# Kernel optimization log

Measured on AMD Instinct MI355X. Metric: run time of the kernel, lower is better.

Reference implementation:

```python
import jax, jax.numpy as jnp
import numpy as np

B, S, IN, HID, HEADS, TRAITS = 128, 32, 32, 128, 8, 10


def setup_inputs() -> dict:
    key = jax.random.key(0)
    ks = jax.random.split(key, 40)
    f32 = jnp.float32
    def W(k, shape, s=0.02):
        return (jax.random.normal(k, shape, f32) * s)
    path = jax.random.normal(ks[0], (B, S, IN), f32)
    # monotonically increasing shared time grid (timestamps[0] is what cdeint uses)
    dt = jax.random.uniform(ks[1], (S,), f32, 0.05, 0.15)
    ts = jnp.broadcast_to(jnp.cumsum(dt), (B, S))
    inp = {
        "interaction_path": path,
        "timestamps": ts,
        # initial encoder: Linear(IN,HID) -> LN -> GELU -> Linear(HID,HID) -> LN
        "enc_W1": W(ks[2], (IN, HID)), "enc_b1": jnp.zeros((HID,), f32),
        "enc_g1": jnp.ones((HID,), f32), "enc_bt1": jnp.zeros((HID,), f32),
        "enc_W2": W(ks[3], (HID, HID)), "enc_b2": jnp.zeros((HID,), f32),
        "enc_g2": jnp.ones((HID,), f32), "enc_bt2": jnp.zeros((HID,), f32),
        # vector field: Linear(HID,2HID)->LN->GELU -> Linear(2HID,2HID)->LN->GELU -> Linear(2HID,HID*IN)
        "vf_W1": W(ks[4], (HID, 2 * HID)), "vf_b1": jnp.zeros((2 * HID,), f32),
        "vf_g1": jnp.ones((2 * HID,), f32), "vf_bt1": jnp.zeros((2 * HID,), f32),
        "vf_W2": W(ks[5], (2 * HID, 2 * HID)), "vf_b2": jnp.zeros((2 * HID,), f32),
        "vf_g2": jnp.ones((2 * HID,), f32), "vf_bt2": jnp.zeros((2 * HID,), f32),
        "vf_W3": W(ks[6], (2 * HID, HID * IN), 0.005), "vf_b3": jnp.zeros((HID * IN,), f32),
        # MultiheadAttention (q=k=v, single token)
        "Wq": W(ks[7], (HID, HID)), "bq": jnp.zeros((HID,), f32),
        "Wk": W(ks[8], (HID, HID)), "bk": jnp.zeros((HID,), f32),
        "Wv": W(ks[9], (HID, HID)), "bv": jnp.zeros((HID,), f32),
        "Wo": W(ks[10], (HID, HID)), "bo": jnp.zeros((HID,), f32),
        # trait decoder (2-layer MLP -> TRAITS)
        "dec_W1": W(ks[11], (HID, HID)), "dec_b1": jnp.zeros((HID,), f32),
        "dec_W2": W(ks[12], (HID, TRAITS)), "dec_b2": jnp.zeros((TRAITS,), f32),
    }
    return inp


def reference(interaction_path, timestamps,
              enc_W1, enc_b1, enc_g1, enc_bt1, enc_W2, enc_b2, enc_g2, enc_bt2,
              vf_W1, vf_b1, vf_g1, vf_bt1, vf_W2, vf_b2, vf_g2, vf_bt2, vf_W3, vf_b3,
              Wq, bq, Wk, bk, Wv, bv, Wo, bo,
              dec_W1, dec_b1, dec_W2, dec_b2):
    b, s, in_dim = interaction_path.shape
    hid = enc_W1.shape[1]
    nh = HEADS
    dh = hid // nh

    def ln(x, g, bb):
        mu = jnp.mean(x, -1, keepdims=True)
        v = jnp.mean((x - mu) ** 2, -1, keepdims=True)
        return (x - mu) / jnp.sqrt(v + 1e-5) * g + bb

    gelu = lambda x: jax.nn.gelu(x, approximate=False)

    # initial encoder on first time point (dropout = eval mode)
    x0 = interaction_path[:, 0]
    h0 = gelu(ln(x0 @ enc_W1 + enc_b1, enc_g1, enc_bt1))
    z0 = ln(h0 @ enc_W2 + enc_b2, enc_g2, enc_bt2)  # [B, HID]

    # linear-interpolation control path: piecewise-constant derivative per interval
    dts = timestamps[:, 1:] - timestamps[:, :-1]                       # [B, S-1]
    dX = (interaction_path[:, 1:] - interaction_path[:, :-1]) / dts[..., None]  # [B, S-1, IN]

    def vf(z):
        h = gelu(ln(z @ vf_W1 + vf_b1, vf_g1, vf_bt1))
        h = gelu(ln(h @ vf_W2 + vf_b2, vf_g2, vf_bt2))
        return (h @ vf_W3 + vf_b3).reshape(z.shape[0], hid, in_dim)    # [B, HID, IN]

    def drift(z, dxdt):
        return jnp.einsum('bhi,bi->bh', vf(z), dxdt)

    def rk4_step(z, inp):
        dxdt, hstep = inp               # [B, IN], [B]
        hb = hstep[:, None]
        k1 = drift(z, dxdt)
        k2 = drift(z + 0.5 * hb * k1, dxdt)
        k3 = drift(z + 0.5 * hb * k2, dxdt)
        k4 = drift(z + hb * k3, dxdt)
        z_next = z + (hb / 6.0) * (k1 + 2 * k2 + 2 * k3 + k4)
        return z_next, None

    zT, _ = jax.lax.scan(rk4_step, z0, (jnp.swapaxes(dX, 0, 1), dts.T))  # [B, HID]

    # single-token self-attention (softmax over one key -> weights = 1)
    q = (zT @ Wq + bq).reshape(b, nh, dh)
    k = (zT @ Wk + bk).reshape(b, nh, dh)
    v = (zT @ Wv + bv).reshape(b, nh, dh)
    scores = jnp.sum(q * k, -1, keepdims=True) / jnp.sqrt(jnp.float32(dh))  # [B, nh, 1]
    w = jax.nn.softmax(scores[..., None], axis=-1)                           # [B, nh, 1, 1] == 1
    attn = (w[..., 0] * v).reshape(b, hid)
    final = attn @ Wo + bo
    attention_weights = jnp.mean(w, axis=1)  # [B, 1, 1] averaged over heads (torch default)

    hD = gelu(final @ dec_W1 + dec_b1)
    traits = hD @ dec_W2 + dec_b2            # [B, TRAITS]
    return traits, attention_weights
```

## Files before the change

kernel.cpp:

```cpp
#include <hip/hip_runtime.h>
#include <hip/hip_bf16.h>

#define BB 128
#define SS 32
#define NSTEP 31
#define IND 32
#define HID 128
#define HID2 256

typedef unsigned short u16;
typedef unsigned int u32;
typedef _Float16 f16;
typedef f16 h2 __attribute__((ext_vector_type(2)));
typedef __fp16 fp16v2 __attribute__((ext_vector_type(2)));
typedef _Float16 f16x8 __attribute__((ext_vector_type(8)));
typedef float f32x4 __attribute__((ext_vector_type(4)));

__device__ __forceinline__ float dot2f(u32 a, u32 b, float c){
#if __has_builtin(__builtin_amdgcn_fdot2)
  h2 ha, hb; __builtin_memcpy(&ha, &a, 4); __builtin_memcpy(&hb, &b, 4);
  return __builtin_amdgcn_fdot2(ha, hb, c, false);
#else
  h2 ha, hb; __builtin_memcpy(&ha, &a, 4); __builtin_memcpy(&hb, &b, 4);
  return c + (float)ha[0]*(float)hb[0] + (float)ha[1]*(float)hb[1];
#endif
}
__device__ __forceinline__ u32 pkh2(float a, float b){
  fp16v2 r = __builtin_amdgcn_cvt_pkrtz(a, b);
  u32 u; __builtin_memcpy(&u, &r, 4); return u;
}
__device__ __forceinline__ u16 f2h(float f){ f16 h = (f16)f; u16 u; __builtin_memcpy(&u, &h, 2); return u; }
__device__ __forceinline__ float gelu_f(float x){ return 0.5f * x * (1.0f + erff(x * 0.70710678118654752440f)); }

__device__ __forceinline__ float wred(float v){
  int iv; float tf;
  #define DPPADD(CTRL, RMASK) \
    __builtin_memcpy(&iv, &v, 4); \
    iv = __builtin_amdgcn_update_dpp(0, iv, CTRL, RMASK, 0xf, true); \
    __builtin_memcpy(&tf, &iv, 4); \
    v += tf;
  DPPADD(0x111, 0xf)
  DPPADD(0x112, 0xf)
  DPPADD(0x114, 0xf)
  DPPADD(0x118, 0xf)
  DPPADD(0x142, 0xa)
  DPPADD(0x143, 0xc)
  #undef DPPADD
  return v;
}

__device__ __forceinline__ void bsum2(float x, float y, float* red, int tid, float& ox, float& oy){
  #pragma unroll
  for (int off = 32; off >= 1; off >>= 1){ x += __shfl_xor(x, off); y += __shfl_xor(y, off); }
  __syncthreads();
  if ((tid & 63) == 0){ red[(tid >> 6)*2] = x; red[(tid >> 6)*2 + 1] = y; }
  __syncthreads();
  ox = red[0] + red[2] + red[4] + red[6];
  oy = red[1] + red[3] + red[5] + red[7];
}

__global__ __launch_bounds__(128) void prep_misc(const float* __restrict__ path,
                                                 const float* __restrict__ ts,
                                                 const float* __restrict__ b3,
                                                 u32* __restrict__ dxh,
                                                 float* __restrict__ hb,
                                                 float* __restrict__ gb){
  const int b = blockIdx.x, tid = threadIdx.x;
  __shared__ float sdx[NSTEP * IND];
  for (int t = tid; t < NSTEP * IND; t += 128){
    int s = t >> 5, i = t & 31;
    float dt = ts[b*SS + s + 1] - ts[b*SS + s];
    sdx[t] = (path[(b*SS + s + 1)*IND + i] - path[(b*SS + s)*IND + i]) / dt;
  }
  if (tid < NSTEP) hb[b*NSTEP + tid] = ts[b*SS + tid + 1] - ts[b*SS + tid];
  __syncthreads();
  for (int t = tid; t < NSTEP * 16; t += 128){
    int s = t >> 4, i2 = t & 15;
    dxh[((size_t)b*NSTEP + s)*16 + i2] = pkh2(sdx[s*IND + 2*i2], sdx[s*IND + 2*i2 + 1]);
  }
  if (tid < HID){
    float w[IND];
    #pragma unroll
    for (int i = 0; i < IND; ++i) w[i] = b3[tid*IND + i];
    for (int s = 0; s < NSTEP; ++s){
      float a = 0.f;
      #pragma unroll
      for (int i = 0; i < IND; ++i) a = fmaf(w[i], sdx[s*IND + i], a);
      gb[(b*NSTEP + s)*HID + tid] = a;
    }
  }
}

__global__ __launch_bounds__(256) void pack_w3(const float* __restrict__ W3, u32* __restrict__ w3h){
  int i = blockIdx.x*256 + threadIdx.x;
  if (i < (HID2*HID*IND)/2) w3h[i] = pkh2(W3[2*i], W3[2*i + 1]);
}

__global__ __launch_bounds__(256) void pack_wf(const float* __restrict__ W1,
                                               const float* __restrict__ W2,
                                               u32* __restrict__ w1f,
                                               u32* __restrict__ w2f){
  int i = blockIdx.x*256 + threadIdx.x;
  if (i < 16384){
    int lane_blk = i >> 6, rem = i & 63;
    int i16 = rem >> 2, q = rem & 3;
    int w = lane_blk >> 6, lane = lane_blk & 63;
    int kt = i16 >> 2, nt = i16 & 3;
    int k = kt*32 + (lane >> 4)*8 + 2*q;
    int col = w*64 + nt*16 + (lane & 15);
    w1f[i] = pkh2(W1[(size_t)k*HID2 + col], W1[(size_t)(k+1)*HID2 + col]);
  } else if (i < 16384 + 32768){
    int j = i - 16384;
    int lane_blk = j >> 7, rem = j & 127;
    int i32i = rem >> 2, q = rem & 3;
    int w = lane_blk >> 6, lane = lane_blk & 63;
    int kt = i32i >> 2, nt = i32i & 3;
    int k = kt*32 + (lane >> 4)*8 + 2*q;
    int col = w*64 + nt*16 + (lane & 15);
    w2f[j] = pkh2(W2[(size_t)k*HID2 + col], W2[(size_t)(k+1)*HID2 + col]);
  }
}

__global__ __launch_bounds__(256) void gprep_h(const u32* __restrict__ w3h,
                                               const u32* __restrict__ dxh,
                                               u32* __restrict__ Gp, int s0){
  const int tid = threadIdx.x;
  const int sl = blockIdx.y; const int s = s0 + sl;
  const int lin = blockIdx.x*256 + tid;
  const int kp = lin >> 7, h = lin & 127;
  const uint4* wa = (const uint4*)(w3h + ((size_t)(2*kp)*HID + h)*16);
  const uint4* wb = (const uint4*)(w3h + ((size_t)(2*kp+1)*HID + h)*16);
  uint4 A0 = wa[0], A1 = wa[1], A2 = wa[2], A3 = wa[3];
  uint4 B0 = wb[0], B1 = wb[1], B2 = wb[2], B3 = wb[3];
  __shared__ u32 sdx[BB * 16];
  for (int t = tid; t < BB * 16; t += 256){
    int bb = t >> 4, i2 = t & 15;
    sdx[t] = dxh[((size_t)bb*NSTEP + s)*16 + i2];
  }
  __syncthreads();
  const int kt = kp >> 4, q = kp & 3, quad2 = (kp >> 2) & 3;
  const int wq = h >> 5, tq = (h >> 4) & 1, nn = h & 15;
  const size_t off = (size_t)wq*4096 + (size_t)(kt*2 + tq)*256 + (size_t)(quad2*16 + nn)*4 + q;
  const size_t base_sl = (size_t)sl * BB * 16384;
  for (int bb = 0; bb < BB; ++bb){
    const uint4* dp = (const uint4*)&sdx[bb*16];
    uint4 D0 = dp[0], D1 = dp[1], D2 = dp[2], D3 = dp[3];
    float g0 = 0.f, g1 = 0.f, g2 = 0.f, g3 = 0.f;
    g0 = dot2f(D0.x, A0.x, g0); g0 = dot2f(D0.y, A0.y, g0);
    g0 = dot2f(D0.z, A0.z, g0); g0 = dot2f(D0.w, A0.w, g0);
    g2 = dot2f(D1.x, A1.x, g2); g2 = dot2f(D1.y, A1.y, g2);
    g2 = dot2f(D1.z, A1.z, g2); g2 = dot2f(D1.w, A1.w, g2);
    g0 = dot2f(D2.x, A2.x, g0); g0 = dot2f(D2.y, A2.y, g0);
    g0 = dot2f(D2.z, A2.z, g0); g0 = dot2f(D2.w, A2.w, g0);
    g2 = dot2f(D3.x, A3.x, g2); g2 = dot2f(D3.y, A3.y, g2);
    g2 = dot2f(D3.z, A3.z, g2); g2 = dot2f(D3.w, A3.w, g2);
    g1 = dot2f(D0.x, B0.x, g1); g1 = dot2f(D0.y, B0.y, g1);
    g1 = dot2f(D0.z, B0.z, g1); g1 = dot2f(D0.w, B0.w, g1);
    g3 = dot2f(D1.x, B1.x, g3); g3 = dot2f(D1.y, B1.y, g3);
    g3 = dot2f(D1.z, B1.z, g3); g3 = dot2f(D1.w, B1.w, g3);
    g1 = dot2f(D2.x, B2.x, g1); g1 = dot2f(D2.y, B2.y, g1);
    g1 = dot2f(D2.z, B2.z, g1); g1 = dot2f(D2.w, B2.w, g1);
    g3 = dot2f(D3.x, B3.x, g3); g3 = dot2f(D3.y, B3.y, g3);
    g3 = dot2f(D3.z, B3.z, g3); g3 = dot2f(D3.w, B3.w, g3);
    Gp[base_sl + (size_t)bb*16384 + off] = pkh2(g0 + g2, g1 + g3);
  }
}

struct ScanP {
  const float *path;
  const float *eW1,*eb1,*eg1,*ebt1,*eW2,*eb2,*eg2,*ebt2;
  const u32 *w1f, *w2f;
  const float *b1,*g1,*bt1,*b2,*g2,*bt2;
  const float *Wv,*bv,*Wo,*bo,*dW1,*db1,*dW2,*db2;
  const float *hb,*gb;
  const u32 *Gp;
  float *zstate, *out;
  int s0, s1, do_enc, do_epi;
};

__global__ __launch_bounds__(256, 1) void scan_kernel(ScanP p){
  const int tid = threadIdx.x;
  const int b = blockIdx.x;
  const int lane = tid & 63, w = tid >> 6;
  const int quad = lane >> 4, n16 = lane & 15;
  const bool owner = (quad == 0);
  __shared__ __align__(16) u16 zst_h[HID];
  __shared__ __align__(16) u16 a1p_h[HID2];
  __shared__ __align__(16) u16 a2p_h[HID2];
  __shared__ __align__(16) float red[8];
  __shared__ __align__(16) float zf[HID];
  __shared__ __align__(16) float sc1[HID2];

  uint4 w1r[16], w2r[32];
  {
    const uint4* s1p = (const uint4*)p.w1f + ((size_t)(w*64 + lane))*16;
    #pragma unroll
    for (int i = 0; i < 16; ++i) w1r[i] = s1p[i];
    const uint4* s2p = (const uint4*)p.w2f + ((size_t)(w*64 + lane))*32;
    #pragma unroll
    for (int i = 0; i < 32; ++i) w2r[i] = s2p[i];
  }
  float rb1[4], rg1[4], rbt1[4], rb2[4], rg2[4], rbt2[4];
  #pragma unroll
  for (int nt = 0; nt < 4; ++nt){
    int col = w*64 + nt*16 + n16;
    rb1[nt] = p.b1[col]; rg1[nt] = p.g1[col]; rbt1[nt] = p.bt1[col];
    rb2[nt] = p.b2[col]; rg2[nt] = p.g2[col]; rbt2[nt] = p.bt2[col];
  }
  const int h0 = w*32 + n16, h1 = h0 + 16;

  float mu, sq;
  if (p.do_enc){
    if (tid < IND) sc1[tid] = p.path[(b*SS + 0)*IND + tid];
    __syncthreads();
    float acc = 0.f;
    if (tid < HID){
      acc = p.eb1[tid];
      #pragma unroll 8
      for (int i = 0; i < IND; ++i) acc = fmaf(sc1[i], p.eW1[i*HID + tid], acc);
    }
    float cx = (tid < HID) ? acc : 0.f;
    bsum2(cx, cx*cx, red, tid, mu, sq);
    mu *= (1.f/HID); float var = sq*(1.f/HID) - mu*mu; float rstd = rsqrtf(var + 1e-5f);
    if (tid < HID) zf[tid] = gelu_f((acc - mu)*rstd*p.eg1[tid] + p.ebt1[tid]);
    __syncthreads();
    float acc2 = 0.f;
    if (tid < HID){
      acc2 = p.eb2[tid];
      #pragma unroll 8
      for (int h = 0; h < HID; ++h) acc2 = fmaf(zf[h], p.eW2[h*HID + tid], acc2);
    }
    cx = (tid < HID) ? acc2 : 0.f;
    bsum2(cx, cx*cx, red, tid, mu, sq);
    mu *= (1.f/HID); float var2 = sq*(1.f/HID) - mu*mu; float rstd2 = rsqrtf(var2 + 1e-5f);
    __syncthreads();
    if (tid < HID) zf[tid] = (acc2 - mu)*rstd2*p.eg2[tid] + p.ebt2[tid];
    __syncthreads();
  }
  float zc0 = 0.f, zc1 = 0.f;
  if (owner){
    if (p.do_enc){ zc0 = zf[h0]; zc1 = zf[h1]; }
    else { zc0 = p.zstate[b*HID + h0]; zc1 = p.zstate[b*HID + h1]; }
  }

  for (int s = p.s0; s < p.s1; ++s){
    const float hbv = p.hb[b*NSTEP + s];
    uint4 gr[16];
    {
      const uint4* g4 = (const uint4*)(p.Gp + ((size_t)(s - p.s0)*BB + b)*16384 + (size_t)w*4096);
      #pragma unroll
      for (int m = 0; m < 16; ++m) gr[m] = g4[m*64 + lane];
    }
    float gb0 = 0.f, gb1 = 0.f;
    if (owner){
      gb0 = p.gb[(b*NSTEP + s)*HID + h0];
      gb1 = p.gb[(b*NSTEP + s)*HID + h1];
      zst_h[h0] = f2h(zc0); zst_h[h1] = f2h(zc1);
    }
    float ks0 = 0.f, ks1 = 0.f;
    __syncthreads();

    #pragma unroll 1
    for (int st = 0; st < 4; ++st){
      f32x4 D0 = {0,0,0,0}, D1 = {0,0,0,0}, D2 = {0,0,0,0}, D3 = {0,0,0,0};
      {
        const uint4* za = (const uint4*)zst_h;
        #pragma unroll
        for (int kt = 0; kt < 4; ++kt){
          f16x8 a; uint4 av = za[kt*4 + quad]; __builtin_memcpy(&a, &av, 16);
          f16x8 bf;
          __builtin_memcpy(&bf, &w1r[kt*4+0], 16); D0 = __builtin_amdgcn_mfma_f32_16x16x32_f16(a, bf, D0, 0, 0, 0);
          __builtin_memcpy(&bf, &w1r[kt*4+1], 16); D1 = __builtin_amdgcn_mfma_f32_16x16x32_f16(a, bf, D1, 0, 0, 0);
          __builtin_memcpy(&bf, &w1r[kt*4+2], 16); D2 = __builtin_amdgcn_mfma_f32_16x16x32_f16(a, bf, D2, 0, 0, 0);
          __builtin_memcpy(&bf, &w1r[kt*4+3], 16); D3 = __builtin_amdgcn_mfma_f32_16x16x32_f16(a, bf, D3, 0, 0, 0);
        }
      }
      float v0 = D0[0] + rb1[0], v1 = D1[0] + rb1[1], v2 = D2[0] + rb1[2], v3 = D3[0] + rb1[3];
      float ssum = wred((v0 + v1) + (v2 + v3));
      float ssq  = wred((v0*v0 + v1*v1) + (v2*v2 + v3*v3));
      if (lane == 63){ red[w*2] = ssum; red[w*2+1] = ssq; }
      __syncthreads();
      {
        const float4* r4 = (const float4*)red;
        float4 ra = r4[0], rb = r4[1];
        float m1 = (ra.x + ra.z + rb.x + rb.z)*(1.f/1024.f);
        float q1 = (ra.y + ra.w + rb.y + rb.w)*(1.f/1024.f);
        float rs1 = rsqrtf(q1 - m1*m1 + 1e-5f);
        if (owner){
          a1p_h[w*64 +  0 + n16] = f2h(gelu_f((v0 - m1)*rs1*rg1[0] + rbt1[0]));
          a1p_h[w*64 + 16 + n16] = f2h(gelu_f((v1 - m1)*rs1*rg1[1] + rbt1[1]));
          a1p_h[w*64 + 32 + n16] = f2h(gelu_f((v2 - m1)*rs1*rg1[2] + rbt1[2]));
          a1p_h[w*64 + 48 + n16] = f2h(gelu_f((v3 - m1)*rs1*rg1[3] + rbt1[3]));
        }
      }
      __syncthreads();
      D0 = {0,0,0,0}; D1 = {0,0,0,0}; D2 = {0,0,0,0}; D3 = {0,0,0,0};
      {
        const uint4* aa = (const uint4*)a1p_h;
        #pragma unroll
        for (int kt = 0; kt < 8; ++kt){
          f16x8 a; uint4 av = aa[kt*4 + quad]; __builtin_memcpy(&a, &av, 16);
          f16x8 bf;
          __builtin_memcpy(&bf, &w2r[kt*4+0], 16); D0 = __builtin_amdgcn_mfma_f32_16x16x32_f16(a, bf, D0, 0, 0, 0);
          __builtin_memcpy(&bf, &w2r[kt*4+1], 16); D1 = __builtin_amdgcn_mfma_f32_16x16x32_f16(a, bf, D1, 0, 0, 0);
          __builtin_memcpy(&bf, &w2r[kt*4+2], 16); D2 = __builtin_amdgcn_mfma_f32_16x16x32_f16(a, bf, D2, 0, 0, 0);
          __builtin_memcpy(&bf, &w2r[kt*4+3], 16); D3 = __builtin_amdgcn_mfma_f32_16x16x32_f16(a, bf, D3, 0, 0, 0);
        }
      }
      v0 = D0[0] + rb2[0]; v1 = D1[0] + rb2[1]; v2 = D2[0] + rb2[2]; v3 = D3[0] + rb2[3];
      ssum = wred((v0 + v1) + (v2 + v3));
      ssq  = wred((v0*v0 + v1*v1) + (v2*v2 + v3*v3));
      if (lane == 63){ red[w*2] = ssum; red[w*2+1] = ssq; }
      __syncthreads();
      {
        const float4* r4 = (const float4*)red;
        float4 ra = r4[0], rb = r4[1];
        float m2 = (ra.x + ra.z + rb.x + rb.z)*(1.f/1024.f);
        float q2 = (ra.y + ra.w + rb.y + rb.w)*(1.f/1024.f);
        float rs2 = rsqrtf(q2 - m2*m2 + 1e-5f);
        if (owner){
          a2p_h[w*64 +  0 + n16] = f2h(gelu_f((v0 - m2)*rs2*rg2[0] + rbt2[0]));
          a2p_h[w*64 + 16 + n16] = f2h(gelu_f((v1 - m2)*rs2*rg2[1] + rbt2[1]));
          a2p_h[w*64 + 32 + n16] = f2h(gelu_f((v2 - m2)*rs2*rg2[2] + rbt2[2]));
          a2p_h[w*64 + 48 + n16] = f2h(gelu_f((v3 - m2)*rs2*rg2[3] + rbt2[3]));
        }
      }
      __syncthreads();
      f32x4 E0 = {0,0,0,0}, E1 = {0,0,0,0};
      {
        const uint4* aa = (const uint4*)a2p_h;
        #pragma unroll
        for (int kt = 0; kt < 8; ++kt){
          f16x8 a; uint4 av = aa[kt*4 + quad]; __builtin_memcpy(&a, &av, 16);
          f16x8 g0f, g1f;
          __builtin_memcpy(&g0f, &gr[kt*2+0], 16);
          __builtin_memcpy(&g1f, &gr[kt*2+1], 16);
          E0 = __builtin_amdgcn_mfma_f32_16x16x32_f16(a, g0f, E0, 0, 0, 0);
          E1 = __builtin_amdgcn_mfma_f32_16x16x32_f16(a, g1f, E1, 0, 0, 0);
        }
      }
      if (owner){
        float kv0 = E0[0] + gb0, kv1 = E1[0] + gb1;
        float cst = (st == 0 || st == 3) ? 1.f : 2.f;
        ks0 += cst*kv0; ks1 += cst*kv1;
        if (st < 3){
          float c = (st == 2) ? hbv : 0.5f*hbv;
          zst_h[h0] = f2h(zc0 + c*kv0);
          zst_h[h1] = f2h(zc1 + c*kv1);
        }
      }
      __syncthreads();
    }
    if (owner){ zc0 += hbv*(1.f/6.f)*ks0; zc1 += hbv*(1.f/6.f)*ks1; }
  }

  if (p.do_epi){
    if (owner){ zf[h0] = zc0; zf[h1] = zc1; }
    __syncthreads();
    if (tid < HID){
      float v = p.bv[tid];
      #pragma unroll 8
      for (int h = 0; h < HID; ++h) v = fmaf(zf[h], p.Wv[h*HID + tid], v);
      sc1[tid] = v;
    }
    __syncthreads();
    if (tid < HID){
      float f = p.bo[tid];
      #pragma unroll 8
      for (int h = 0; h < HID; ++h) f = fmaf(sc1[h], p.Wo[h*HID + tid], f);
      sc1[HID + tid] = f;
    }
    __syncthreads();
    if (tid < HID){
      float hd = p.db1[tid];
      #pragma unroll 8
      for (int h = 0; h < HID; ++h) hd = fmaf(sc1[HID + h], p.dW1[h*HID + tid], hd);
      zf[tid] = gelu_f(hd);
    }
    __syncthreads();
    if (tid < 10){
      float t = p.db2[tid];
      #pragma unroll 8
      for (int h = 0; h < HID; ++h) t = fmaf(zf[h], p.dW2[h*10 + tid], t);
      p.out[b*10 + tid] = t;
    }
    if (tid == 0) p.out[BB*10 + b] = 1.0f;
  } else {
    if (owner){ p.zstate[b*HID + h0] = zc0; p.zstate[b*HID + h1] = zc1; }
  }
}

extern "C" void kernel_launch(void* const* d_in, const int* in_sizes, int n_in,
                              void* d_out, int out_size, void* d_ws, size_t ws_size,
                              hipStream_t stream){
  const float* path  = (const float*)d_in[0];
  const float* ts    = (const float*)d_in[1];
  const float* eW1   = (const float*)d_in[2];
  const float* eb1   = (const float*)d_in[3];
  const float* eg1   = (const float*)d_in[4];
  const float* ebt1  = (const float*)d_in[5];
  const float* eW2   = (const float*)d_in[6];
  const float* eb2   = (const float*)d_in[7];
  const float* eg2   = (const float*)d_in[8];
  const float* ebt2  = (const float*)d_in[9];
  const float* vW1   = (const float*)d_in[10];
  const float* vb1   = (const float*)d_in[11];
  const float* vg1   = (const float*)d_in[12];
  const float* vbt1  = (const float*)d_in[13];
  const float* vW2   = (const float*)d_in[14];
  const float* vb2   = (const float*)d_in[15];
  const float* vg2   = (const float*)d_in[16];
  const float* vbt2  = (const float*)d_in[17];
  const float* vW3   = (const float*)d_in[18];
  const float* vb3   = (const float*)d_in[19];
  const float* Wv    = (const float*)d_in[24];
  const float* bv    = (const float*)d_in[25];
  const float* Wo    = (const float*)d_in[26];
  const float* bo    = (const float*)d_in[27];
  const float* dW1   = (const float*)d_in[28];
  const float* db1   = (const float*)d_in[29];
  const float* dW2   = (const float*)d_in[30];
  const float* db2   = (const float*)d_in[31];

  char* wsb = (char*)d_ws;
  float* z_state = (float*)(wsb + 0);
  u32*   dxh = (u32*)(wsb + 65536);
  float* hb  = (float*)(wsb + 319488);
  float* gb  = (float*)(wsb + 335872);
  u32*   w3h = (u32*)(wsb + 2367488);
  u32*   w1f = (u32*)(wsb + 4464640);
  u32*   w2f = (u32*)(wsb + 4530176);
  u32*   Gp  = (u32*)(wsb + 4661248);

  hipLaunchKernelGGL(prep_misc, dim3(BB), dim3(128), 0, stream, path, ts, vb3, dxh, hb, gb);
  hipLaunchKernelGGL(pack_w3, dim3(2048), dim3(256), 0, stream, vW3, w3h);
  hipLaunchKernelGGL(pack_wf, dim3(192), dim3(256), 0, stream, vW1, vW2, w1f, w2f);

  const size_t per_step = (size_t)BB * 16384 * 4;
  size_t gav = (ws_size > 4661248) ? (ws_size - 4661248) : per_step;
  int chunk = (int)(gav / per_step);
  if (chunk < 1) chunk = 1;
  if (chunk > NSTEP) chunk = NSTEP;

  for (int s0 = 0; s0 < NSTEP; s0 += chunk){
    int cs = (NSTEP - s0 < chunk) ? (NSTEP - s0) : chunk;
    hipLaunchKernelGGL(gprep_h, dim3(64, cs), dim3(256), 0, stream, w3h, dxh, Gp, s0);
    ScanP P;
    P.path = path;
    P.eW1 = eW1; P.eb1 = eb1; P.eg1 = eg1; P.ebt1 = ebt1;
    P.eW2 = eW2; P.eb2 = eb2; P.eg2 = eg2; P.ebt2 = ebt2;
    P.w1f = w1f; P.w2f = w2f;
    P.b1 = vb1; P.g1 = vg1; P.bt1 = vbt1;
    P.b2 = vb2; P.g2 = vg2; P.bt2 = vbt2;
    P.Wv = Wv; P.bv = bv; P.Wo = Wo; P.bo = bo;
    P.dW1 = dW1; P.db1 = db1; P.dW2 = dW2; P.db2 = db2;
    P.hb = hb; P.gb = gb; P.Gp = Gp;
    P.zstate = z_state; P.out = (float*)d_out;
    P.s0 = s0; P.s1 = s0 + cs;
    P.do_enc = (s0 == 0) ? 1 : 0;
    P.do_epi = (s0 + cs == NSTEP) ? 1 : 0;
    hipLaunchKernelGGL(scan_kernel, dim3(BB), dim3(256), 0, stream, P);
  }
}
```

Baseline: 608.6 us.

## Batch four samples per scan block to fill MFMA rows

The scan kernel now handles four batch elements per block (32 blocks instead of 128). The fp16 MFMA A-operand rows carry four samples instead of one, so the vector-field MLP layers and LayerNorm reductions are shared across samples. Each wave also owns one sample for the G-matrix contraction, with software-prefetched G loads. The encoder moves to MFMA using newly packed weights, and the gprep output layout is simplified to a linear fragment order. The trade-off is far fewer blocks (32 on a large GPU), so much less parallelism, plus a serialised per-sample epilogue.

```diff
diff --git a/kernel.cpp b/kernel.cpp
--- a/kernel.cpp
+++ b/kernel.cpp
@@ -2,11 +2,15 @@
 #include <hip/hip_bf16.h>
 
 #define BB 128
+#define BPB 4
+#define NBLK 32
 #define SS 32
 #define NSTEP 31
 #define IND 32
 #define HID 128
 #define HID2 256
+#define BSTR 272
+#define ZSTR 136
 
 typedef unsigned short u16;
 typedef unsigned int u32;
@@ -32,31 +36,16 @@
 __device__ __forceinline__ u16 f2h(float f){ f16 h = (f16)f; u16 u; __builtin_memcpy(&u, &h, 2); return u; }
 __device__ __forceinline__ float gelu_f(float x){ return 0.5f * x * (1.0f + erff(x * 0.70710678118654752440f)); }
 
-__device__ __forceinline__ float wred(float v){
+__device__ __forceinline__ float dpp16sum(float v){
   int iv; float tf;
-  #define DPPADD(CTRL, RMASK) \
+  #define DPPADD(CTRL) \
     __builtin_memcpy(&iv, &v, 4); \
-    iv = __builtin_amdgcn_update_dpp(0, iv, CTRL, RMASK, 0xf, true); \
+    iv = __builtin_amdgcn_update_dpp(0, iv, CTRL, 0xf, 0xf, true); \
     __builtin_memcpy(&tf, &iv, 4); \
     v += tf;
-  DPPADD(0x111, 0xf)
-  DPPADD(0x112, 0xf)
-  DPPADD(0x114, 0xf)
-  DPPADD(0x118, 0xf)
-  DPPADD(0x142, 0xa)
-  DPPADD(0x143, 0xc)
+  DPPADD(0x111) DPPADD(0x112) DPPADD(0x114) DPPADD(0x118)
   #undef DPPADD
   return v;
-}
-
-__device__ __forceinline__ void bsum2(float x, float y, float* red, int tid, float& ox, float& oy){
-  #pragma unroll
-  for (int off = 32; off >= 1; off >>= 1){ x += __shfl_xor(x, off); y += __shfl_xor(y, off); }
-  __syncthreads();
-  if ((tid & 63) == 0){ red[(tid >> 6)*2] = x; red[(tid >> 6)*2 + 1] = y; }
-  __syncthreads();
-  ox = red[0] + red[2] + red[4] + red[6];
-  oy = red[1] + red[3] + red[5] + red[7];
 }
 
 __global__ __launch_bounds__(128) void prep_misc(const float* __restrict__ path,
@@ -98,8 +87,12 @@
 
 __global__ __launch_bounds__(256) void pack_wf(const float* __restrict__ W1,
                                                const float* __restrict__ W2,
+                                               const float* __restrict__ EW1,
+                                               const float* __restrict__ EW2,
                                                u32* __restrict__ w1f,
-                                               u32* __restrict__ w2f){
+                                               u32* __restrict__ w2f,
+                                               u32* __restrict__ w1e,
+                                               u32* __restrict__ w2e){
   int i = blockIdx.x*256 + threadIdx.x;
   if (i < 16384){
     int lane_blk = i >> 6, rem = i & 63;
@@ -109,7 +102,7 @@
     int k = kt*32 + (lane >> 4)*8 + 2*q;
     int col = w*64 + nt*16 + (lane & 15);
     w1f[i] = pkh2(W1[(size_t)k*HID2 + col], W1[(size_t)(k+1)*HID2 + col]);
-  } else if (i < 16384 + 32768){
+  } else if (i < 49152){
     int j = i - 16384;
     int lane_blk = j >> 7, rem = j & 127;
     int i32i = rem >> 2, q = rem & 3;
@@ -118,6 +111,18 @@
     int k = kt*32 + (lane >> 4)*8 + 2*q;
     int col = w*64 + nt*16 + (lane & 15);
     w2f[j] = pkh2(W2[(size_t)k*HID2 + col], W2[(size_t)(k+1)*HID2 + col]);
+  } else if (i < 51200){
+    int u = i - 49152;
+    int q = u & 3, nf = (u>>2) & 1, lane = (u>>3) & 63, w = u >> 9;
+    int k = (lane >> 4)*8 + 2*q;
+    int col = w*32 + nf*16 + (lane & 15);
+    w1e[u] = pkh2(EW1[(size_t)k*HID + col], EW1[(size_t)(k+1)*HID + col]);
+  } else if (i < 59392){
+    int u = i - 51200;
+    int q = u & 3, nf = (u>>2) & 1, kt = (u>>3) & 3, lane = (u>>5) & 63, w = u >> 11;
+    int k = kt*32 + (lane >> 4)*8 + 2*q;
+    int col = w*32 + nf*16 + (lane & 15);
+    w2e[u] = pkh2(EW2[(size_t)k*HID + col], EW2[(size_t)(k+1)*HID + col]);
   }
 }
 
@@ -126,10 +131,12 @@
                                                u32* __restrict__ Gp, int s0){
   const int tid = threadIdx.x;
   const int sl = blockIdx.y; const int s = s0 + sl;
-  const int lin = blockIdx.x*256 + tid;
-  const int kp = lin >> 7, h = lin & 127;
-  const uint4* wa = (const uint4*)(w3h + ((size_t)(2*kp)*HID + h)*16);
-  const uint4* wb = (const uint4*)(w3h + ((size_t)(2*kp+1)*HID + h)*16);
+  const int o = blockIdx.x*256 + tid;
+  const int q = o & 3, lane = (o>>2) & 63, nf = (o>>8) & 7, kt = o >> 11;
+  const int k0 = kt*32 + (lane >> 4)*8 + 2*q;
+  const int h = nf*16 + (lane & 15);
+  const uint4* wa = (const uint4*)(w3h + ((size_t)k0*HID + h)*16);
+  const uint4* wb = (const uint4*)(w3h + ((size_t)(k0+1)*HID + h)*16);
   uint4 A0 = wa[0], A1 = wa[1], A2 = wa[2], A3 = wa[3];
   uint4 B0 = wb[0], B1 = wb[1], B2 = wb[2], B3 = wb[3];
   __shared__ u32 sdx[BB * 16];
@@ -138,9 +145,6 @@
     sdx[t] = dxh[((size_t)bb*NSTEP + s)*16 + i2];
   }
   __syncthreads();
-  const int kt = kp >> 4, q = kp & 3, quad2 = (kp >> 2) & 3;
-  const int wq = h >> 5, tq = (h >> 4) & 1, nn = h & 15;
-  const size_t off = (size_t)wq*4096 + (size_t)(kt*2 + tq)*256 + (size_t)(quad2*16 + nn)*4 + q;
   const size_t base_sl = (size_t)sl * BB * 16384;
   for (int bb = 0; bb < BB; ++bb){
     const uint4* dp = (const uint4*)&sdx[bb*16];
@@ -162,13 +166,14 @@
     g1 = dot2f(D2.z, B2.z, g1); g1 = dot2f(D2.w, B2.w, g1);
     g3 = dot2f(D3.x, B3.x, g3); g3 = dot2f(D3.y, B3.y, g3);
     g3 = dot2f(D3.z, B3.z, g3); g3 = dot2f(D3.w, B3.w, g3);
-    Gp[base_sl + (size_t)bb*16384 + off] = pkh2(g0 + g2, g1 + g3);
+    Gp[base_sl + (size_t)bb*16384 + o] = pkh2(g0 + g2, g1 + g3);
   }
 }
 
 struct ScanP {
   const float *path;
-  const float *eW1,*eb1,*eg1,*ebt1,*eW2,*eb2,*eg2,*ebt2;
+  const u32 *w1e, *w2e;
+  const float *eb1,*eg1,*ebt1,*eb2,*eg2,*ebt2;
   const u32 *w1f, *w2f;
   const float *b1,*g1,*bt1,*b2,*g2,*bt2;
   const float *Wv,*bv,*Wo,*bo,*dW1,*db1,*dW2,*db2;
@@ -180,16 +185,18 @@
 
 __global__ __launch_bounds__(256, 1) void scan_kernel(ScanP p){
   const int tid = threadIdx.x;
-  const int b = blockIdx.x;
+  const int b0 = blockIdx.x * BPB;
   const int lane = tid & 63, w = tid >> 6;
-  const int quad = lane >> 4, n16 = lane & 15;
+  const int quad = lane >> 4, n16 = lane & 15, bl = n16 & 3;
   const bool owner = (quad == 0);
-  __shared__ __align__(16) u16 zst_h[HID];
-  __shared__ __align__(16) u16 a1p_h[HID2];
-  __shared__ __align__(16) u16 a2p_h[HID2];
-  __shared__ __align__(16) float red[8];
-  __shared__ __align__(16) float zf[HID];
-  __shared__ __align__(16) float sc1[HID2];
+
+  __shared__ __align__(16) u16 bufA[BPB*BSTR];
+  __shared__ __align__(16) u16 bufB[BPB*BSTR];
+  __shared__ __align__(16) u16 zsth[BPB*ZSTR];
+  __shared__ __align__(16) float redl[32];
+  __shared__ __align__(16) float zf[BPB*HID];
+  __shared__ __align__(16) float e1[HID];
+  __shared__ __align__(16) float e2[HID];
 
   uint4 w1r[16], w2r[32];
   {
@@ -202,191 +209,312 @@
   }
   float rb1[4], rg1[4], rbt1[4], rb2[4], rg2[4], rbt2[4];
   #pragma unroll
-  for (int nt = 0; nt < 4; ++nt){
-    int col = w*64 + nt*16 + n16;
-    rb1[nt] = p.b1[col]; rg1[nt] = p.g1[col]; rbt1[nt] = p.bt1[col];
-    rb2[nt] = p.b2[col]; rg2[nt] = p.g2[col]; rbt2[nt] = p.bt2[col];
-  }
-  const int h0 = w*32 + n16, h1 = h0 + 16;
-
-  float mu, sq;
+  for (int nf = 0; nf < 4; ++nf){
+    int col = w*64 + nf*16 + n16;
+    rb1[nf] = p.b1[col]; rg1[nf] = p.g1[col]; rbt1[nf] = p.bt1[col];
+    rb2[nf] = p.b2[col]; rg2[nf] = p.g2[col]; rbt2[nf] = p.bt2[col];
+  }
+
+  float zc[8];
+
   if (p.do_enc){
-    if (tid < IND) sc1[tid] = p.path[(b*SS + 0)*IND + tid];
+    uint4 e1r[2], e2r[8];
+    {
+      const uint4* q1 = (const uint4*)p.w1e + ((size_t)(w*64 + lane))*2;
+      e1r[0] = q1[0]; e1r[1] = q1[1];
+      const uint4* q2 = (const uint4*)p.w2e + ((size_t)(w*64 + lane))*8;
+      #pragma unroll
+      for (int i = 0; i < 8; ++i) e2r[i] = q2[i];
+    }
+    float ec1b[2],ec1g[2],ec1t[2],ec2b[2],ec2g[2],ec2t[2];
+    #pragma unroll
+    for (int nf = 0; nf < 2; ++nf){
+      int colE = w*32 + nf*16 + n16;
+      ec1b[nf]=p.eb1[colE]; ec1g[nf]=p.eg1[colE]; ec1t[nf]=p.ebt1[colE];
+      ec2b[nf]=p.eb2[colE]; ec2g[nf]=p.eg2[colE]; ec2t[nf]=p.ebt2[colE];
+    }
+    f16x8 ax;
+    {
+      const float4* xp = (const float4*)(p.path + ((size_t)(b0+bl)*SS)*IND + quad*8);
+      float4 xa = xp[0], xb = xp[1];
+      u32 pk4[4] = { pkh2(xa.x,xa.y), pkh2(xa.z,xa.w), pkh2(xb.x,xb.y), pkh2(xb.z,xb.w) };
+      __builtin_memcpy(&ax, pk4, 16);
+    }
+    f32x4 D0={0,0,0,0}, D1={0,0,0,0};
+    { f16x8 bf;
+      __builtin_memcpy(&bf, &e1r[0], 16); D0 = __builtin_amdgcn_mfma_f32_16x16x32_f16(ax, bf, D0, 0, 0, 0);
+      __builtin_memcpy(&bf, &e1r[1], 16); D1 = __builtin_amdgcn_mfma_f32_16x16x32_f16(ax, bf, D1, 0, 0, 0); }
+    float v0[2][4];
+    #pragma unroll
+    for (int i = 0; i < 4; ++i){ v0[0][i] = D0[i] + ec1b[0]; v0[1][i] = D1[i] + ec1b[1]; }
+    {
+      float sm[4], sqv[4];
+      #pragma unroll
+      for (int i = 0; i < 4; ++i){
+        sm[i]  = dpp16sum(v0[0][i] + v0[1][i]);
+        sqv[i] = dpp16sum(v0[0][i]*v0[0][i] + v0[1][i]*v0[1][i]);
+      }
+      if (lane == 15){
+        ((float4*)redl)[w*2]   = make_float4(sm[0], sqv[0], sm[1], sqv[1]);
+        ((float4*)redl)[w*2+1] = make_float4(sm[2], sqv[2], sm[3], sqv[3]);
+      }
+      __syncthreads();
+      const float4* r4 = (const float4*)redl;
+      float4 r0=r4[0], r1=r4[1], r2=r4[2], r3=r4[3], r5=r4[4], r6=r4[5], r7=r4[6], r8=r4[7];
+      float ms[4], rs[4];
+      ms[0]=((r0.x+r2.x)+(r5.x+r7.x))*(1.f/HID); float q0=((r0.y+r2.y)+(r5.y+r7.y))*(1.f/HID);
+      ms[1]=((r0.z+r2.z)+(r5.z+r7.z))*(1.f/HID); float q1=((r0.w+r2.w)+(r5.w+r7.w))*(1.f/HID);
+      ms[2]=((r1.x+r3.x)+(r6.x+r8.x))*(1.f/HID); float q2=((r1.y+r3.y)+(r6.y+r8.y))*(1.f/HID);
+      ms[3]=((r1.z+r3.z)+(r6.z+r8.z))*(1.f/HID); float q3=((r1.w+r3.w)+(r6.w+r8.w))*(1.f/HID);
+      rs[0]=rsqrtf(q0-ms[0]*ms[0]+1e-5f); rs[1]=rsqrtf(q1-ms[1]*ms[1]+1e-5f);
+      rs[2]=rsqrtf(q2-ms[2]*ms[2]+1e-5f); rs[3]=rsqrtf(q3-ms[3]*ms[3]+1e-5f);
+      if (owner){
+        #pragma unroll
+        for (int nf = 0; nf < 2; ++nf)
+          #pragma unroll
+          for (int i = 0; i < 4; ++i)
+            zsth[i*ZSTR + w*32 + nf*16 + n16] = f2h(gelu_f((v0[nf][i]-ms[i])*rs[i]*ec1g[nf] + ec1t[nf]));
+      }
+    }
     __syncthreads();
-    float acc = 0.f;
-    if (tid < HID){
-      acc = p.eb1[tid];
-      #pragma unroll 8
-      for (int i = 0; i < IND; ++i) acc = fmaf(sc1[i], p.eW1[i*HID + tid], acc);
-    }
-    float cx = (tid < HID) ? acc : 0.f;
-    bsum2(cx, cx*cx, red, tid, mu, sq);
-    mu *= (1.f/HID); float var = sq*(1.f/HID) - mu*mu; float rstd = rsqrtf(var + 1e-5f);
-    if (tid < HID) zf[tid] = gelu_f((acc - mu)*rstd*p.eg1[tid] + p.ebt1[tid]);
+    f32x4 E0={0,0,0,0}, E1={0,0,0,0};
+    #pragma unroll
+    for (int kt = 0; kt < 4; ++kt){
+      f16x8 a; uint4 av = ((const uint4*)zsth)[bl*17 + kt*4 + quad]; __builtin_memcpy(&a, &av, 16);
+      f16x8 bf;
+      __builtin_memcpy(&bf, &e2r[kt*2+0], 16); E0 = __builtin_amdgcn_mfma_f32_16x16x32_f16(a, bf, E0, 0, 0, 0);
+      __builtin_memcpy(&bf, &e2r[kt*2+1], 16); E1 = __builtin_amdgcn_mfma_f32_16x16x32_f16(a, bf, E1, 0, 0, 0);
+    }
+    #pragma unroll
+    for (int i = 0; i < 4; ++i){ v0[0][i] = E0[i] + ec2b[0]; v0[1][i] = E1[i] + ec2b[1]; }
+    {
+      float sm[4], sqv[4];
+      #pragma unroll
+      for (int i = 0; i < 4; ++i){
+        sm[i]  = dpp16sum(v0[0][i] + v0[1][i]);
+        sqv[i] = dpp16sum(v0[0][i]*v0[0][i] + v0[1][i]*v0[1][i]);
+      }
+      if (lane == 15){
+        ((float4*)redl)[w*2]   = make_float4(sm[0], sqv[0], sm[1], sqv[1]);
+        ((float4*)redl)[w*2+1] = make_float4(sm[2], sqv[2], sm[3], sqv[3]);
+      }
+      __syncthreads();
+      const float4* r4 = (const float4*)redl;
+      float4 r0=r4[0], r1=r4[1], r2=r4[2], r3=r4[3], r5=r4[4], r6=r4[5], r7=r4[6], r8=r4[7];
+      float ms[4], rs[4];
+      ms[0]=((r0.x+r2.x)+(r5.x+r7.x))*(1.f/HID); float q0=((r0.y+r2.y)+(r5.y+r7.y))*(1.f/HID);
+      ms[1]=((r0.z+r2.z)+(r5.z+r7.z))*(1.f/HID); float q1=((r0.w+r2.w)+(r5.w+r7.w))*(1.f/HID);
+      ms[2]=((r1.x+r3.x)+(r6.x+r8.x))*(1.f/HID); float q2=((r1.y+r3.y)+(r6.y+r8.y))*(1.f/HID);
+      ms[3]=((r1.z+r3.z)+(r6.z+r8.z))*(1.f/HID); float q3=((r1.w+r3.w)+(r6.w+r8.w))*(1.f/HID);
+      rs[0]=rsqrtf(q0-ms[0]*ms[0]+1e-5f); rs[1]=rsqrtf(q1-ms[1]*ms[1]+1e-5f);
+      rs[2]=rsqrtf(q2-ms[2]*ms[2]+1e-5f); rs[3]=rsqrtf(q3-ms[3]*ms[3]+1e-5f);
+      if (owner){
+        #pragma unroll
+        for (int nf = 0; nf < 2; ++nf)
+          #pragma unroll
+          for (int i = 0; i < 4; ++i)
+            zf[i*HID + w*32 + nf*16 + n16] = (v0[nf][i]-ms[i])*rs[i]*ec2g[nf] + ec2t[nf];
+      }
+    }
     __syncthreads();
-    float acc2 = 0.f;
-    if (tid < HID){
-      acc2 = p.eb2[tid];
-      #pragma unroll 8
-      for (int h = 0; h < HID; ++h) acc2 = fmaf(zf[h], p.eW2[h*HID + tid], acc2);
-    }
-    cx = (tid < HID) ? acc2 : 0.f;
-    bsum2(cx, cx*cx, red, tid, mu, sq);
-    mu *= (1.f/HID); float var2 = sq*(1.f/HID) - mu*mu; float rstd2 = rsqrtf(var2 + 1e-5f);
-    __syncthreads();
-    if (tid < HID) zf[tid] = (acc2 - mu)*rstd2*p.eg2[tid] + p.ebt2[tid];
-    __syncthreads();
-  }
-  float zc0 = 0.f, zc1 = 0.f;
-  if (owner){
-    if (p.do_enc){ zc0 = zf[h0]; zc1 = zf[h1]; }
-    else { zc0 = p.zstate[b*HID + h0]; zc1 = p.zstate[b*HID + h1]; }
-  }
-
-  for (int s = p.s0; s < p.s1; ++s){
-    const float hbv = p.hb[b*NSTEP + s];
-    uint4 gr[16];
-    {
-      const uint4* g4 = (const uint4*)(p.Gp + ((size_t)(s - p.s0)*BB + b)*16384 + (size_t)w*4096);
-      #pragma unroll
-      for (int m = 0; m < 16; ++m) gr[m] = g4[m*64 + lane];
-    }
-    float gb0 = 0.f, gb1 = 0.f;
+    #pragma unroll
+    for (int nf = 0; nf < 8; ++nf) zc[nf] = zf[w*HID + nf*16 + n16];
+  } else {
+    #pragma unroll
+    for (int nf = 0; nf < 8; ++nf) zc[nf] = p.zstate[(size_t)(b0+w)*HID + nf*16 + n16];
+  }
+
+  const int nsteps = p.s1 - p.s0;
+  #pragma unroll 1
+  for (int sl = 0; sl < nsteps; ++sl){
+    const int s = p.s0 + sl;
+    const float hbv = p.hb[(b0+w)*NSTEP + s];
+    float gbv[8];
+    #pragma unroll
+    for (int nf = 0; nf < 8; ++nf) gbv[nf] = p.gb[((size_t)(b0+w)*NSTEP + s)*HID + nf*16 + n16];
     if (owner){
-      gb0 = p.gb[(b*NSTEP + s)*HID + h0];
-      gb1 = p.gb[(b*NSTEP + s)*HID + h1];
-      zst_h[h0] = f2h(zc0); zst_h[h1] = f2h(zc1);
-    }
-    float ks0 = 0.f, ks1 = 0.f;
+      #pragma unroll
+      for (int nf = 0; nf < 8; ++nf) zsth[w*ZSTR + nf*16 + n16] = f2h(zc[nf]);
+    }
+    float ks[8];
+    #pragma unroll
+    for (int nf = 0; nf < 8; ++nf) ks[nf] = 0.f;
+    const uint4* g4 = (const uint4*)(p.Gp + ((size_t)sl*BB + b0 + w)*16384);
     __syncthreads();
 
     #pragma unroll 1
     for (int st = 0; st < 4; ++st){
-      f32x4 D0 = {0,0,0,0}, D1 = {0,0,0,0}, D2 = {0,0,0,0}, D3 = {0,0,0,0};
+      f32x4 D[4];
+      #pragma unroll
+      for (int nf = 0; nf < 4; ++nf) D[nf] = (f32x4){0,0,0,0};
+      #pragma unroll
+      for (int kt = 0; kt < 4; ++kt){
+        f16x8 a; uint4 av = ((const uint4*)zsth)[bl*17 + kt*4 + quad]; __builtin_memcpy(&a, &av, 16);
+        #pragma unroll
+        for (int nf = 0; nf < 4; ++nf){
+          f16x8 bf; __builtin_memcpy(&bf, &w1r[kt*4+nf], 16);
+          D[nf] = __builtin_amdgcn_mfma_f32_16x16x32_f16(a, bf, D[nf], 0, 0, 0);
+        }
+      }
+      float v[4][4];
+      #pragma unroll
+      for (int nf = 0; nf < 4; ++nf)
+        #pragma unroll
+        for (int i = 0; i < 4; ++i) v[nf][i] = D[nf][i] + rb1[nf];
+      float ms[4], rs[4];
       {
-        const uint4* za = (const uint4*)zst_h;
-        #pragma unroll
-        for (int kt = 0; kt < 4; ++kt){
-          f16x8 a; uint4 av = za[kt*4 + quad]; __builtin_memcpy(&a, &av, 16);
-          f16x8 bf;
-          __builtin_memcpy(&bf, &w1r[kt*4+0], 16); D0 = __builtin_amdgcn_mfma_f32_16x16x32_f16(a, bf, D0, 0, 0, 0);
-          __builtin_memcpy(&bf, &w1r[kt*4+1], 16); D1 = __builtin_amdgcn_mfma_f32_16x16x32_f16(a, bf, D1, 0, 0, 0);
-          __builtin_memcpy(&bf, &w1r[kt*4+2], 16); D2 = __builtin_amdgcn_mfma_f32_16x16x32_f16(a, bf, D2, 0, 0, 0);
-          __builtin_memcpy(&bf, &w1r[kt*4+3], 16); D3 = __builtin_amdgcn_mfma_f32_16x16x32_f16(a, bf, D3, 0, 0, 0);
-        }
-      }
-      float v0 = D0[0] + rb1[0], v1 = D1[0] + rb1[1], v2 = D2[0] + rb1[2], v3 = D3[0] + rb1[3];
-      float ssum = wred((v0 + v1) + (v2 + v3));
-      float ssq  = wred((v0*v0 + v1*v1) + (v2*v2 + v3*v3));
-      if (lane == 63){ red[w*2] = ssum; red[w*2+1] = ssq; }
-      __syncthreads();
+        float sm[4], sqv[4];
+        #pragma unroll
+        for (int i = 0; i < 4; ++i){
+          sm[i]  = dpp16sum((v[0][i]+v[1][i]) + (v[2][i]+v[3][i]));
+          sqv[i] = dpp16sum((v[0][i]*v[0][i]+v[1][i]*v[1][i]) + (v[2][i]*v[2][i]+v[3][i]*v[3][i]));
+        }
+        if (lane == 15){
+          ((float4*)redl)[w*2]   = make_float4(sm[0], sqv[0], sm[1], sqv[1]);
+          ((float4*)redl)[w*2+1] = make_float4(sm[2], sqv[2], sm[3], sqv[3]);
+        }
+        __syncthreads();
+        const float4* r4 = (const float4*)redl;
+        float4 r0=r4[0], r1=r4[1], r2=r4[2], r3=r4[3], r5=r4[4], r6=r4[5], r7=r4[6], r8=r4[7];
+        ms[0]=((r0.x+r2.x)+(r5.x+r7.x))*(1.f/HID2); float q0=((r0.y+r2.y)+(r5.y+r7.y))*(1.f/HID2);
+        ms[1]=((r0.z+r2.z)+(r5.z+r7.z))*(1.f/HID2); float q1=((r0.w+r2.w)+(r5.w+r7.w))*(1.f/HID2);
+        ms[2]=((r1.x+r3.x)+(r6.x+r8.x))*(1.f/HID2); float q2=((r1.y+r3.y)+(r6.y+r8.y))*(1.f/HID2);
+        ms[3]=((r1.z+r3.z)+(r6.z+r8.z))*(1.f/HID2); float q3=((r1.w+r3.w)+(r6.w+r8.w))*(1.f/HID2);
+        rs[0]=rsqrtf(q0-ms[0]*ms[0]+1e-5f); rs[1]=rsqrtf(q1-ms[1]*ms[1]+1e-5f);
+        rs[2]=rsqrtf(q2-ms[2]*ms[2]+1e-5f); rs[3]=rsqrtf(q3-ms[3]*ms[3]+1e-5f);
+      }
+      if (owner){
+        #pragma unroll
+        for (int nf = 0; nf < 4; ++nf)
+          #pragma unroll
+          for (int i = 0; i < 4; ++i)
+            bufA[i*BSTR + w*64 + nf*16 + n16] = f2h(gelu_f((v[nf][i]-ms[i])*rs[i]*rg1[nf] + rbt1[nf]));
+      }
+      __syncthreads();
+      #pragma unroll
+      for (int nf = 0; nf < 4; ++nf) D[nf] = (f32x4){0,0,0,0};
+      #pragma unroll
+      for (int kt = 0; kt < 8; ++kt){
+        f16x8 a; uint4 av = ((const uint4*)bufA)[bl*34 + kt*4 + quad]; __builtin_memcpy(&a, &av, 16);
+        #pragma unroll
+        for (int nf = 0; nf < 4; ++nf){
+          f16x8 bf; __builtin_memcpy(&bf, &w2r[kt*4+nf], 16);
+          D[nf] = __builtin_amdgcn_mfma_f32_16x16x32_f16(a, bf, D[nf], 0, 0, 0);
+        }
+      }
+      #pragma unroll
+      for (int nf = 0; nf < 4; ++nf)
+        #pragma unroll
+        for (int i = 0; i < 4; ++i) v[nf][i] = D[nf][i] + rb2[nf];
       {
-        const float4* r4 = (const float4*)red;
-        float4 ra = r4[0], rb = r4[1];
-        float m1 = (ra.x + ra.z + rb.x + rb.z)*(1.f/1024.f);
-        float q1 = (ra.y + ra.w + rb.y + rb.w)*(1.f/1024.f);
-        float rs1 = rsqrtf(q1 - m1*m1 + 1e-5f);
-        if (owner){
-          a1p_h[w*64 +  0 + n16] = f2h(gelu_f((v0 - m1)*rs1*rg1[0] + rbt1[0]));
-          a1p_h[w*64 + 16 + n16] = f2h(gelu_f((v1 - m1)*rs1*rg1[1] + rbt1[1]));
-          a1p_h[w*64 + 32 + n16] = f2h(gelu_f((v2 - m1)*rs1*rg1[2] + rbt1[2]));
-          a1p_h[w*64 + 48 + n16] = f2h(gelu_f((v3 - m1)*rs1*rg1[3] + rbt1[3]));
-        }
-      }
-      __syncthreads();
-      D0 = {0,0,0,0}; D1 = {0,0,0,0}; D2 = {0,0,0,0}; D3 = {0,0,0,0};
-      {
-        const uint4* aa = (const uint4*)a1p_h;
-        #pragma unroll
-        for (int kt = 0; kt < 8; ++kt){
-          f16x8 a; uint4 av = aa[kt*4 + quad]; __builtin_memcpy(&a, &av, 16);
-          f16x8 bf;
-          __builtin_memcpy(&bf, &w2r[kt*4+0], 16); D0 = __builtin_amdgcn_mfma_f32_16x16x32_f16(a, bf, D0, 0, 0, 0);
-          __builtin_memcpy(&bf, &w2r[kt*4+1], 16); D1 = __builtin_amdgcn_mfma_f32_16x16x32_f16(a, bf, D1, 0, 0, 0);
-          __builtin_memcpy(&bf, &w2r[kt*4+2], 16); D2 = __builtin_amdgcn_mfma_f32_16x16x32_f16(a, bf, D2, 0, 0, 0);
-          __builtin_memcpy(&bf, &w2r[kt*4+3], 16); D3 = __builtin_amdgcn_mfma_f32_16x16x32_f16(a, bf, D3, 0, 0, 0);
-        }
-      }
-      v0 = D0[0] + rb2[0]; v1 = D1[0] + rb2[1]; v2 = D2[0] + rb2[2]; v3 = D3[0] + rb2[3];
-      ssum = wred((v0 + v1) + (v2 + v3));
-      ssq  = wred((v0*v0 + v1*v1) + (v2*v2 + v3*v3));
-      if (lane == 63){ red[w*2] = ssum; red[w*2+1] = ssq; }
-      __syncthreads();
-      {
-        const float4* r4 = (const float4*)red;
-        float4 ra = r4[0], rb = r4[1];
-        float m2 = (ra.x + ra.z + rb.x + rb.z)*(1.f/1024.f);
-        float q2 = (ra.y + ra.w + rb.y + rb.w)*(1.f/1024.f);
-        float rs2 = rsqrtf(q2 - m2*m2 + 1e-5f);
-        if (owner){
-          a2p_h[w*64 +  0 + n16] = f2h(gelu_f((v0 - m2)*rs2*rg2[0] + rbt2[0]));
-          a2p_h[w*64 + 16 + n16] = f2h(gelu_f((v1 - m2)*rs2*rg2[1] + rbt2[1]));
-          a2p_h[w*64 + 32 + n16] = f2h(gelu_f((v2 - m2)*rs2*rg2[2] + rbt2[2]));
-          a2p_h[w*64 + 48 + n16] = f2h(gelu_f((v3 - m2)*rs2*rg2[3] + rbt2[3]));
-        }
-      }
-      __syncthreads();
-      f32x4 E0 = {0,0,0,0}, E1 = {0,0,0,0};
-      {
-        const uint4* aa = (const uint4*)a2p_h;
-        #pragma unroll
-        for (int kt = 0; kt < 8; ++kt){
-          f16x8 a; uint4 av = aa[kt*4 + quad]; __builtin_memcpy(&a, &av, 16);
-          f16x8 g0f, g1f;
-          __builtin_memcpy(&g0f, &gr[kt*2+0], 16);
-          __builtin_memcpy(&g1f, &gr[kt*2+1], 16);
-          E0 = __builtin_amdgcn_mfma_f32_16x16x32_f16(a, g0f, E0, 0, 0, 0);
-          E1 = __builtin_amdgcn_mfma_f32_16x16x32_f16(a, g1f, E1, 0, 0, 0);
-        }
+        float sm[4], sqv[4];
+        #pragma unroll
+        for (int i = 0; i < 4; ++i){
+          sm[i]  = dpp16sum((v[0][i]+v[1][i]) + (v[2][i]+v[3][i]));
+          sqv[i] = dpp16sum((v[0][i]*v[0][i]+v[1][i]*v[1][i]) + (v[2][i]*v[2][i]+v[3][i]*v[3][i]));
+        }
+        if (lane == 15){
+          ((float4*)redl)[w*2]   = make_float4(sm[0], sqv[0], sm[1], sqv[1]);
+          ((float4*)redl)[w*2+1] = make_float4(sm[2], sqv[2], sm[3], sqv[3]);
+        }
+        __syncthreads();
+        const float4* r4 = (const float4*)redl;
+        float4 r0=r4[0], r1=r4[1], r2=r4[2], r3=r4[3], r5=r4[4], r6=r4[5], r7=r4[6], r8=r4[7];
+        ms[0]=((r0.x+r2.x)+(r5.x+r7.x))*(1.f/HID2); float q0=((r0.y+r2.y)+(r5.y+r7.y))*(1.f/HID2);
+        ms[1]=((r0.z+r2.z)+(r5.z+r7.z))*(1.f/HID2); float q1=((r0.w+r2.w)+(r5.w+r7.w))*(1.f/HID2);
+        ms[2]=((r1.x+r3.x)+(r6.x+r8.x))*(1.f/HID2); float q2=((r1.y+r3.y)+(r6.y+r8.y))*(1.f/HID2);
+        ms[3]=((r1.z+r3.z)+(r6.z+r8.z))*(1.f/HID2); float q3=((r1.w+r3.w)+(r6.w+r8.w))*(1.f/HID2);
+        rs[0]=rsqrtf(q0-ms[0]*ms[0]+1e-5f); rs[1]=rsqrtf(q1-ms[1]*ms[1]+1e-5f);
+        rs[2]=rsqrtf(q2-ms[2]*ms[2]+1e-5f); rs[3]=rsqrtf(q3-ms[3]*ms[3]+1e-5f);
       }
       if (owner){
-        float kv0 = E0[0] + gb0, kv1 = E1[0] + gb1;
-        float cst = (st == 0 || st == 3) ? 1.f : 2.f;
-        ks0 += cst*kv0; ks1 += cst*kv1;
-        if (st < 3){
-          float c = (st == 2) ? hbv : 0.5f*hbv;
-          zst_h[h0] = f2h(zc0 + c*kv0);
-          zst_h[h1] = f2h(zc1 + c*kv1);
-        }
-      }
-      __syncthreads();
-    }
-    if (owner){ zc0 += hbv*(1.f/6.f)*ks0; zc1 += hbv*(1.f/6.f)*ks1; }
+        #pragma unroll
+        for (int nf = 0; nf < 4; ++nf)
+          #pragma unroll
+          for (int i = 0; i < 4; ++i)
+            bufB[i*BSTR + w*64 + nf*16 + n16] = f2h(gelu_f((v[nf][i]-ms[i])*rs[i]*rg2[nf] + rbt2[nf]));
+      }
+      __syncthreads();
+      f32x4 E[8];
+      #pragma unroll
+      for (int nf = 0; nf < 8; ++nf) E[nf] = (f32x4){0,0,0,0};
+      uint4 ga[8], gn[8];
+      #pragma unroll
+      for (int nf = 0; nf < 8; ++nf) ga[nf] = g4[nf*64 + lane];
+      #pragma unroll
+      for (int kt = 0; kt < 8; ++kt){
+        if (kt < 7){
+          #pragma unroll
+          for (int nf = 0; nf < 8; ++nf) gn[nf] = g4[((kt+1)*8 + nf)*64 + lane];
+        }
+        f16x8 a; uint4 av = ((const uint4*)bufB)[w*34 + kt*4 + quad]; __builtin_memcpy(&a, &av, 16);
+        #pragma unroll
+        for (int nf = 0; nf < 8; ++nf){
+          f16x8 gf; __builtin_memcpy(&gf, &ga[nf], 16);
+          E[nf] = __builtin_amdgcn_mfma_f32_16x16x32_f16(a, gf, E[nf], 0, 0, 0);
+        }
+        if (kt < 7){
+          #pragma unroll
+          for (int nf = 0; nf < 8; ++nf) ga[nf] = gn[nf];
+        }
+      }
+      const float c1 = (st == 0 || st == 3) ? 1.f : 2.f;
+      const float cz = (st == 2) ? hbv : 0.5f*hbv;
+      #pragma unroll
+      for (int nf = 0; nf < 8; ++nf){
+        float kv = E[nf][0] + gbv[nf];
+        ks[nf] += c1*kv;
+        if (st < 3 && owner) zsth[w*ZSTR + nf*16 + n16] = f2h(zc[nf] + cz*kv);
+      }
+      __syncthreads();
+    }
+    #pragma unroll
+    for (int nf = 0; nf < 8; ++nf) zc[nf] += hbv*(1.f/6.f)*ks[nf];
   }
 
   if (p.do_epi){
-    if (owner){ zf[h0] = zc0; zf[h1] = zc1; }
+    if (owner){
+      #pragma unroll
+      for (int nf = 0; nf < 8; ++nf) zf[w*HID + nf*16 + n16] = zc[nf];
+    }
     __syncthreads();
-    if (tid < HID){
-      float v = p.bv[tid];
-      #pragma unroll 8
-      for (int h = 0; h < HID; ++h) v = fmaf(zf[h], p.Wv[h*HID + tid], v);
-      sc1[tid] = v;
-    }
-    __syncthreads();
-    if (tid < HID){
-      float f = p.bo[tid];
-      #pragma unroll 8
-      for (int h = 0; h < HID; ++h) f = fmaf(sc1[h], p.Wo[h*HID + tid], f);
-      sc1[HID + tid] = f;
-    }
-    __syncthreads();
-    if (tid < HID){
-      float hd = p.db1[tid];
-      #pragma unroll 8
-      for (int h = 0; h < HID; ++h) hd = fmaf(sc1[HID + h], p.dW1[h*HID + tid], hd);
-      zf[tid] = gelu_f(hd);
-    }
-    __syncthreads();
-    if (tid < 10){
-      float t = p.db2[tid];
-      #pragma unroll 8
-      for (int h = 0; h < HID; ++h) t = fmaf(zf[h], p.dW2[h*10 + tid], t);
-      p.out[b*10 + tid] = t;
-    }
-    if (tid == 0) p.out[BB*10 + b] = 1.0f;
+    #pragma unroll 1
+    for (int blq = 0; blq < BPB; ++blq){
+      if (tid < HID){
+        float v = p.bv[tid];
+        #pragma unroll 8
+        for (int h = 0; h < HID; ++h) v = fmaf(zf[blq*HID + h], p.Wv[h*HID + tid], v);
+        e1[tid] = v;
+      }
+      __syncthreads();
+      if (tid < HID){
+        float f = p.bo[tid];
+        #pragma unroll 8
+        for (int h = 0; h < HID; ++h) f = fmaf(e1[h], p.Wo[h*HID + tid], f);
+        e2[tid] = f;
+      }
+      __syncthreads();
+      if (tid < HID){
+        float hd = p.db1[tid];
+        #pragma unroll 8
+        for (int h = 0; h < HID; ++h) hd = fmaf(e2[h], p.dW1[h*HID + tid], hd);
+        e1[tid] = gelu_f(hd);
+      }
+      __syncthreads();
+      if (tid < 10){
+        float t = p.db2[tid];
+        #pragma unroll 8
+        for (int h = 0; h < HID; ++h) t = fmaf(e1[h], p.dW2[h*10 + tid], t);
+        p.out[(b0+blq)*10 + tid] = t;
+      }
+      if (tid == 0) p.out[BB*10 + b0 + blq] = 1.0f;
+      __syncthreads();
+    }
   } else {
-    if (owner){ p.zstate[b*HID + h0] = zc0; p.zstate[b*HID + h1] = zc1; }
+    if (owner){
+      #pragma unroll
+      for (int nf = 0; nf < 8; ++nf) p.zstate[(size_t)(b0+w)*HID + nf*16 + n16] = zc[nf];
+    }
   }
 }
 
@@ -430,14 +558,17 @@
   u32*   w3h = (u32*)(wsb + 2367488);
   u32*   w1f = (u32*)(wsb + 4464640);
   u32*   w2f = (u32*)(wsb + 4530176);
-  u32*   Gp  = (u32*)(wsb + 4661248);
+  u32*   w1e = (u32*)(wsb + 4661248);
+  u32*   w2e = (u32*)(wsb + 4669440);
+  u32*   Gp  = (u32*)(wsb + 4702208);
 
   hipLaunchKernelGGL(prep_misc, dim3(BB), dim3(128), 0, stream, path, ts, vb3, dxh, hb, gb);
   hipLaunchKernelGGL(pack_w3, dim3(2048), dim3(256), 0, stream, vW3, w3h);
-  hipLaunchKernelGGL(pack_wf, dim3(192), dim3(256), 0, stream, vW1, vW2, w1f, w2f);
+  hipLaunchKernelGGL(pack_wf, dim3(232), dim3(256), 0, stream, vW1, vW2, eW1, eW2, w1f, w2f, w1e, w2e);
 
   const size_t per_step = (size_t)BB * 16384 * 4;
-  size_t gav = (ws_size > 4661248) ? (ws_size - 4661248) : per_step;
+  const size_t gbase = 4702208;
+  size_t gav = (ws_size > gbase) ? (ws_size - gbase) : per_step;
   int chunk = (int)(gav / per_step);
   if (chunk < 1) chunk = 1;
   if (chunk > NSTEP) chunk = NSTEP;
@@ -447,8 +578,9 @@
     hipLaunchKernelGGL(gprep_h, dim3(64, cs), dim3(256), 0, stream, w3h, dxh, Gp, s0);
     ScanP P;
     P.path = path;
-    P.eW1 = eW1; P.eb1 = eb1; P.eg1 = eg1; P.ebt1 = ebt1;
-    P.eW2 = eW2; P.eb2 = eb2; P.eg2 = eg2; P.ebt2 = ebt2;
+    P.w1e = w1e; P.w2e = w2e;
+    P.eb1 = eb1; P.eg1 = eg1; P.ebt1 = ebt1;
+    P.eb2 = eb2; P.eg2 = eg2; P.ebt2 = ebt2;
     P.w1f = w1f; P.w2f = w2f;
     P.b1 = vb1; P.g1 = vg1; P.bt1 = vbt1;
     P.b2 = vb2; P.g2 = vg2; P.bt2 = vbt2;
@@ -459,6 +591,6 @@
     P.s0 = s0; P.s1 = s0 + cs;
     P.do_enc = (s0 == 0) ? 1 : 0;
     P.do_epi = (s0 + cs == NSTEP) ? 1 : 0;
-    hipLaunchKernelGGL(scan_kernel, dim3(BB), dim3(256), 0, stream, P);
-  }
-}
+    hipLaunchKernelGGL(scan_kernel, dim3(NBLK), dim3(256), 0, stream, P);
+  }
+}
```

New measurement: 1.360 ms. 2.23x slower.
